# Kernel optimization log

Hardware: AMD Instinct MI355X
Metric: run time of the kernel (lower is better)

## Reference

```python
import jax, jax.numpy as jnp
import numpy as np

N_NODES = 100000
N_EDGES = 600000
DIM = 128
NUM_RELS = 8


def setup_inputs() -> dict:
    key = jax.random.key(0)
    k_x, k_ei, k_et, k_w, k_root = jax.random.split(key, 5)
    x = jax.random.normal(k_x, (N_NODES, DIM), dtype=jnp.float32)
    edge_index = jax.random.randint(k_ei, (2, N_EDGES), 0, N_NODES, dtype=jnp.int64)
    edge_type = jax.random.randint(k_et, (N_EDGES,), 0, NUM_RELS, dtype=jnp.int64)
    # per-relation weights, root weight, bias (as in PyG RGCNConv defaults)
    W = jax.random.normal(k_w, (NUM_RELS, DIM, DIM), dtype=jnp.float32) * 0.05
    W_root = jax.random.normal(k_root, (DIM, DIM), dtype=jnp.float32) * 0.05
    bias = jnp.zeros((DIM,), dtype=jnp.float32)
    return {"x": x, "W": W, "W_root": W_root, "bias": bias,
            "edge_index": edge_index, "edge_type": edge_type}


def reference(x, W, W_root, bias, edge_index, edge_type):
    """RGCNConv (num_bases=None, aggr='mean'):
    out[i] = x[i] @ W_root + bias + sum_r mean_{j in N_r(i)} (x[j] @ W[r])
    """
    src = edge_index[0]
    dst = edge_index[1]
    n = x.shape[0]
    num_rels = W.shape[0]
    x_j = x[src]  # [E, D] gather of source-node features
    out = x @ W_root + bias  # root/self transform
    for r in range(num_rels):  # small fixed relation count
        m = (edge_type == r).astype(x.dtype)  # [E]
        msg = (x_j @ W[r]) * m[:, None]  # [E, D] masked per-relation messages
        agg = jax.ops.segment_sum(msg, dst, num_segments=n)  # [N, D]
        cnt = jax.ops.segment_sum(m, dst, num_segments=n)  # [N]
        out = out + agg / jnp.maximum(cnt, 1.0)[:, None]  # per-relation mean
    return out
```

## Files before the change

kernel.cpp:

```cpp
#include <hip/hip_runtime.h>

#define N_NODES 100000
#define N_EDGES 600000
#define DIM 128
#define NUM_RELS 8
#define NBINS (NUM_RELS * N_NODES)
#define SCAN_NB ((NBINS + 1023) / 1024)
#define XBLOCKS 6250
#define TBLOCKS 576
#define HBLOCKS ((N_EDGES + 255) / 256)

typedef unsigned int u32;
typedef __attribute__((ext_vector_type(8))) short bf16x8;
typedef __attribute__((ext_vector_type(4))) float f32x4;

__device__ __forceinline__ u32 pack2_bf16_rn(float lo, float hi) {
    u32 a = __float_as_uint(lo);
    u32 b = __float_as_uint(hi);
    a += 0x7fffu + ((a >> 16) & 1u);
    b += 0x7fffu + ((b >> 16) & 1u);
    return (a >> 16) | (b & 0xffff0000u);
}

__global__ __launch_bounds__(256) void prep(
    const float* __restrict__ x, uint4* __restrict__ x_bf,
    const float* __restrict__ W, const float* __restrict__ W_root,
    unsigned short* __restrict__ Wt,
    const int* __restrict__ ei, const int* __restrict__ et,
    u32* __restrict__ hist, u32* __restrict__ rank) {
    int b = blockIdx.x, tid = threadIdx.x;
    if (b < XBLOCKS) {
        int t = b * 256 + tid;
        const float4* p = reinterpret_cast<const float4*>(x) + (size_t)t * 2;
        float4 v0 = p[0], v1 = p[1];
        uint4 o;
        o.x = pack2_bf16_rn(v0.x, v0.y);
        o.y = pack2_bf16_rn(v0.z, v0.w);
        o.z = pack2_bf16_rn(v1.x, v1.y);
        o.w = pack2_bf16_rn(v1.z, v1.w);
        x_bf[t] = o;
    } else if (b < XBLOCKS + TBLOCKS) {
        int t = (b - XBLOCKS) * 256 + tid;
        int c  = t >> 14;
        int kn = t & 16383;
        int k = kn >> 7, n = kn & 127;
        float v = (c == 0) ? W_root[kn] : W[(size_t)(c - 1) * DIM * DIM + kn];
        u32 bb = __float_as_uint(v);
        bb += 0x7fffu + ((bb >> 16) & 1u);
        Wt[(size_t)c * 16384 + n * 128 + k] = (unsigned short)(bb >> 16);
    } else {
        int e = (b - XBLOCKS - TBLOCKS) * 256 + tid;
        if (e < N_EDGES) {
            int dst = ei[N_EDGES + e];
            int r   = et[e];
            rank[e] = atomicAdd(&hist[(size_t)dst * NUM_RELS + r], 1u);
        }
    }
}

__global__ __launch_bounds__(256) void scan1(const u32* __restrict__ hist,
                                             u32* __restrict__ bsum) {
    __shared__ u32 sh[256];
    int t = threadIdx.x;
    size_t base = (size_t)blockIdx.x * 1024 + t * 4;
    u32 s = 0;
#pragma unroll
    for (int j = 0; j < 4; ++j) { size_t i = base + j; if (i < NBINS) s += hist[i]; }
    sh[t] = s; __syncthreads();
    for (int off = 128; off > 0; off >>= 1) {
        if (t < off) sh[t] += sh[t + off];
        __syncthreads();
    }
    if (t == 0) bsum[blockIdx.x] = sh[0];
}

__global__ __launch_bounds__(256) void scan2(u32* __restrict__ bsum, int nb) {
    __shared__ u32 sh[256];
    int t = threadIdx.x;
    u32 v[4]; u32 s = 0;
#pragma unroll
    for (int j = 0; j < 4; ++j) { int i = t * 4 + j; v[j] = (i < nb) ? bsum[i] : 0; s += v[j]; }
    sh[t] = s; __syncthreads();
    for (int off = 1; off < 256; off <<= 1) {
        u32 add = (t >= off) ? sh[t - off] : 0;
        __syncthreads();
        sh[t] += add;
        __syncthreads();
    }
    u32 run = (t > 0) ? sh[t - 1] : 0;
#pragma unroll
    for (int j = 0; j < 4; ++j) { int i = t * 4 + j; if (i < nb) bsum[i] = run; run += v[j]; }
}

__global__ __launch_bounds__(256) void scan3(const u32* __restrict__ hist,
                                             const u32* __restrict__ bsum,
                                             u32* __restrict__ starts) {
    __shared__ u32 sh[256];
    int t = threadIdx.x;
    size_t base = (size_t)blockIdx.x * 1024 + t * 4;
    u32 v[4]; u32 s = 0;
#pragma unroll
    for (int j = 0; j < 4; ++j) { size_t i = base + j; v[j] = (i < NBINS) ? hist[i] : 0; s += v[j]; }
    sh[t] = s; __syncthreads();
    for (int off = 1; off < 256; off <<= 1) {
        u32 add = (t >= off) ? sh[t - off] : 0;
        __syncthreads();
        sh[t] += add;
        __syncthreads();
    }
    u32 run = bsum[blockIdx.x] + ((t > 0) ? sh[t - 1] : 0);
#pragma unroll
    for (int j = 0; j < 4; ++j) {
        size_t i = base + j;
        if (i < NBINS) {
            starts[i] = run;
            if (i == NBINS - 1) starts[NBINS] = run + v[j];
            run += v[j];
        }
    }
}

__global__ __launch_bounds__(256) void reorder(const int* __restrict__ ei,
                                               const int* __restrict__ et,
                                               const u32* __restrict__ starts,
                                               const u32* __restrict__ rank,
                                               u32* __restrict__ spk) {
    int e = blockIdx.x * 256 + threadIdx.x;
    if (e >= N_EDGES) return;
    int dst = ei[N_EDGES + e];
    int r   = et[e];
    u32 bin = (u32)((dst & 31) * NUM_RELS + r);
    spk[starts[(size_t)dst * NUM_RELS + r] + rank[e]] = (u32)ei[e] | (bin << 17);
}

#define FLUSH2() do { \
    float sc_ = __builtin_amdgcn_rcpf((float)rcnt); \
    ACC[(u32)cur_bin * 64u + ((((lane >> 2) ^ (((u32)cur_bin >> 3) & 15u)) << 2) | (u32)(lane & 3))] = \
        pack2_bf16_rn(a0 * sc_, a1 * sc_); \
} while (0)

__global__ __launch_bounds__(512, 4) void rgcn_fused(
    const u32*  __restrict__ x32,
    const uint4* __restrict__ x16,
    const uint4* __restrict__ Wt,
    const u32*  __restrict__ starts,
    const u32*  __restrict__ spk,
    const float* __restrict__ bias,
    float* __restrict__ out) {
    extern __shared__ u32 ACC[];
    const int tid = threadIdx.x, w = tid >> 6, lane = tid & 63;
    const int g = lane >> 4, m = lane & 15;
    const int rowbase = blockIdx.x * 32;

    uint4* az = reinterpret_cast<uint4*>(ACC);
#pragma unroll
    for (int i = 0; i < 8; ++i) az[tid + i * 512] = make_uint4(0u, 0u, 0u, 0u);
    __syncthreads();

    {
        const u32 elo = starts[(size_t)blockIdx.x * 256 + w * 32];
        const u32 ehi = starts[(size_t)blockIdx.x * 256 + w * 32 + 32];
        int cur_bin = -1, rcnt = 0;
        float a0 = 0.f, a1 = 0.f;
        for (u32 base = elo; base < ehi; base += 64) {
            const int bn = min(64, (int)(ehi - base));
            u32 pk = 0;
            if (lane < bn) pk = spk[base + lane];
            for (int j0 = 0; j0 < bn; j0 += 8) {
                const int lim = bn - j0;
                u32 v[8];
#pragma unroll
                for (int q = 0; q < 8; ++q) {
                    u32 p = (u32)__shfl((int)pk, j0 + (q < lim ? q : 0));
                    v[q] = x32[(size_t)(p & 0x1FFFFu) * 64 + lane];
                }
#pragma unroll
                for (int q = 0; q < 8; ++q) {
                    if (q < lim) {
                        const u32 p = (u32)__shfl((int)pk, j0 + q);
                        const int b = (int)(p >> 17);
                        if (b != cur_bin) {
                            if (rcnt > 0) FLUSH2();
                            cur_bin = b; a0 = 0.f; a1 = 0.f; rcnt = 0;
                        }
                        const u32 vv = v[q];
                        a0 += __uint_as_float(vv << 16);
                        a1 += __uint_as_float(vv & 0xffff0000u);
                        ++rcnt;
                    }
                }
            }
        }
        if (rcnt > 0) FLUSH2();
    }
    __syncthreads();

    const uint4* ATq = reinterpret_cast<const uint4*>(ACC);
    f32x4 accv[2];
    accv[0] = (f32x4)0.f; accv[1] = (f32x4)0.f;
    union { uint4 u; bf16x8 h; } av, bv;
    const int colg = w * 16 + m;

#pragma unroll
    for (int ks = 0; ks < 4; ++ks) {
        bv.u = Wt[(size_t)colg * 16 + ks * 4 + g];
        bf16x8 bf = bv.h;
#pragma unroll
        for (int mt = 0; mt < 2; ++mt) {
            av.u = x16[(size_t)(rowbase + mt * 16 + m) * 16 + ks * 4 + g];
            accv[mt] = __builtin_amdgcn_mfma_f32_16x16x32_bf16(av.h, bf, accv[mt], 0, 0, 0);
        }
    }

#pragma unroll 1
    for (int r = 0; r < 8; ++r) {
        const uint4* Wc = Wt + (size_t)(r + 1) * 2048;
#pragma unroll
        for (int ks = 0; ks < 4; ++ks) {
            bv.u = Wc[(size_t)colg * 16 + ks * 4 + g];
            bf16x8 bf = bv.h;
#pragma unroll
            for (int mt = 0; mt < 2; ++mt) {
                av.u = ATq[(size_t)((mt * 16 + m) * 8 + r) * 16 + (u32)((ks * 4 + g) ^ m)];
                accv[mt] = __builtin_amdgcn_mfma_f32_16x16x32_bf16(av.h, bf, accv[mt], 0, 0, 0);
            }
        }
    }

    {
        const float bb = bias[colg];
#pragma unroll
        for (int mt = 0; mt < 2; ++mt)
#pragma unroll
            for (int j = 0; j < 4; ++j)
                out[(size_t)(rowbase + mt * 16 + g * 4 + j) * DIM + colg] = accv[mt][j] + bb;
    }
}

extern "C" void kernel_launch(void* const* d_in, const int* in_sizes, int n_in,
                              void* d_out, int out_size, void* d_ws, size_t ws_size,
                              hipStream_t stream) {
    const float* x      = (const float*)d_in[0];
    const float* W      = (const float*)d_in[1];
    const float* W_root = (const float*)d_in[2];
    const float* bias   = (const float*)d_in[3];
    const int*   ei     = (const int*)d_in[4];
    const int*   et     = (const int*)d_in[5];
    float* out = (float*)d_out;

    char* ws = (char*)d_ws;
    uint4*          x_bf   = (uint4*)(ws);
    unsigned short* Wt     = (unsigned short*)(ws + 25600000);
    u32*            starts = (u32*)(ws + 25894912);
    u32*            hist   = (u32*)(ws + 29094928);
    u32*            bsum   = (u32*)(ws + 32294928);
    u32*            rank   = (u32*)(ws + 32299024);
    u32*            spk    = (u32*)(ws + 34699024);

    hipMemsetAsync(hist, 0, (size_t)NBINS * 4, stream);
    prep<<<XBLOCKS + TBLOCKS + HBLOCKS, 256, 0, stream>>>(x, x_bf, W, W_root, Wt, ei, et, hist, rank);
    scan1<<<SCAN_NB, 256, 0, stream>>>(hist, bsum);
    scan2<<<1, 256, 0, stream>>>(bsum, SCAN_NB);
    scan3<<<SCAN_NB, 256, 0, stream>>>(hist, bsum, starts);
    reorder<<<HBLOCKS, 256, 0, stream>>>(ei, et, starts, rank, spk);
    rgcn_fused<<<N_NODES / 32, 512, 65536, stream>>>((const u32*)x_bf, x_bf, (const uint4*)Wt,
                                                     starts, spk, bias, out);
}
```

Before: 230.3 us.

## Halve rows per fused block, merge scan passes, and compute bin starts lazily

The fused aggregation and GEMM kernel now handles 16 rows per block instead of 32. This halves its LDS footprint and lets the launch bounds ask for 8 waves per SIMD, so more blocks can be resident to hide the gather latency. The three-pass scan becomes two: local prefixes plus block sums are written once, and consumers add the block offset on the fly, which removes the separate starts pass and one full read of the histogram. In exchange, each block does half the MFMA work per W fetch, and reorder and the block prologue each do an extra lookup.

```diff
diff --git a/kernel.cpp b/kernel.cpp
--- a/kernel.cpp
+++ b/kernel.cpp
@@ -9,6 +9,11 @@
 #define XBLOCKS 6250
 #define TBLOCKS 576
 #define HBLOCKS ((N_EDGES + 255) / 256)
+
+#define RPB 16
+#define BPB (RPB * NUM_RELS)
+#define FBLOCKS (N_NODES / RPB)
+#define LDS_BYTES ((BPB * 64 + 132) * 4)
 
 typedef unsigned int u32;
 typedef __attribute__((ext_vector_type(8))) short bf16x8;
@@ -58,23 +63,33 @@
     }
 }
 
-__global__ __launch_bounds__(256) void scan1(const u32* __restrict__ hist,
+__global__ __launch_bounds__(256) void scanA(const u32* __restrict__ hist,
+                                             u32* __restrict__ locpre,
                                              u32* __restrict__ bsum) {
     __shared__ u32 sh[256];
     int t = threadIdx.x;
     size_t base = (size_t)blockIdx.x * 1024 + t * 4;
-    u32 s = 0;
-#pragma unroll
-    for (int j = 0; j < 4; ++j) { size_t i = base + j; if (i < NBINS) s += hist[i]; }
+    u32 v[4]; u32 s = 0;
+#pragma unroll
+    for (int j = 0; j < 4; ++j) { size_t i = base + j; v[j] = (i < NBINS) ? hist[i] : 0; s += v[j]; }
     sh[t] = s; __syncthreads();
-    for (int off = 128; off > 0; off >>= 1) {
-        if (t < off) sh[t] += sh[t + off];
-        __syncthreads();
-    }
-    if (t == 0) bsum[blockIdx.x] = sh[0];
-}
-
-__global__ __launch_bounds__(256) void scan2(u32* __restrict__ bsum, int nb) {
+    for (int off = 1; off < 256; off <<= 1) {
+        u32 add = (t >= off) ? sh[t - off] : 0;
+        __syncthreads();
+        sh[t] += add;
+        __syncthreads();
+    }
+    u32 run = (t > 0) ? sh[t - 1] : 0;
+#pragma unroll
+    for (int j = 0; j < 4; ++j) {
+        size_t i = base + j;
+        if (i < NBINS) locpre[i] = run;
+        run += v[j];
+    }
+    if (t == 255) bsum[blockIdx.x] = sh[255];
+}
+
+__global__ __launch_bounds__(256) void scanB(u32* __restrict__ bsum, int nb) {
     __shared__ u32 sh[256];
     int t = threadIdx.x;
     u32 v[4]; u32 s = 0;
@@ -92,45 +107,20 @@
     for (int j = 0; j < 4; ++j) { int i = t * 4 + j; if (i < nb) bsum[i] = run; run += v[j]; }
 }
 
-__global__ __launch_bounds__(256) void scan3(const u32* __restrict__ hist,
-                                             const u32* __restrict__ bsum,
-                                             u32* __restrict__ starts) {
-    __shared__ u32 sh[256];
-    int t = threadIdx.x;
-    size_t base = (size_t)blockIdx.x * 1024 + t * 4;
-    u32 v[4]; u32 s = 0;
-#pragma unroll
-    for (int j = 0; j < 4; ++j) { size_t i = base + j; v[j] = (i < NBINS) ? hist[i] : 0; s += v[j]; }
-    sh[t] = s; __syncthreads();
-    for (int off = 1; off < 256; off <<= 1) {
-        u32 add = (t >= off) ? sh[t - off] : 0;
-        __syncthreads();
-        sh[t] += add;
-        __syncthreads();
-    }
-    u32 run = bsum[blockIdx.x] + ((t > 0) ? sh[t - 1] : 0);
-#pragma unroll
-    for (int j = 0; j < 4; ++j) {
-        size_t i = base + j;
-        if (i < NBINS) {
-            starts[i] = run;
-            if (i == NBINS - 1) starts[NBINS] = run + v[j];
-            run += v[j];
-        }
-    }
-}
-
 __global__ __launch_bounds__(256) void reorder(const int* __restrict__ ei,
                                                const int* __restrict__ et,
-                                               const u32* __restrict__ starts,
+                                               const u32* __restrict__ locpre,
+                                               const u32* __restrict__ bsumx,
                                                const u32* __restrict__ rank,
                                                u32* __restrict__ spk) {
     int e = blockIdx.x * 256 + threadIdx.x;
     if (e >= N_EDGES) return;
     int dst = ei[N_EDGES + e];
     int r   = et[e];
-    u32 bin = (u32)((dst & 31) * NUM_RELS + r);
-    spk[starts[(size_t)dst * NUM_RELS + r] + rank[e]] = (u32)ei[e] | (bin << 17);
+    size_t key = (size_t)dst * NUM_RELS + r;
+    u32 pos = locpre[key] + bsumx[key >> 10] + rank[e];
+    u32 bin = (u32)((dst & (RPB - 1)) * NUM_RELS + r);
+    spk[pos] = (u32)ei[e] | (bin << 17);
 }
 
 #define FLUSH2() do { \
@@ -139,27 +129,33 @@
         pack2_bf16_rn(a0 * sc_, a1 * sc_); \
 } while (0)
 
-__global__ __launch_bounds__(512, 4) void rgcn_fused(
+__global__ __launch_bounds__(512, 8) void rgcn_fused(
     const u32*  __restrict__ x32,
     const uint4* __restrict__ x16,
     const uint4* __restrict__ Wt,
-    const u32*  __restrict__ starts,
+    const u32*  __restrict__ locpre,
+    const u32*  __restrict__ bsumx,
     const u32*  __restrict__ spk,
     const float* __restrict__ bias,
     float* __restrict__ out) {
     extern __shared__ u32 ACC[];
+    u32* BND = ACC + BPB * 64;
     const int tid = threadIdx.x, w = tid >> 6, lane = tid & 63;
     const int g = lane >> 4, m = lane & 15;
-    const int rowbase = blockIdx.x * 32;
+    const int rowbase = blockIdx.x * RPB;
 
     uint4* az = reinterpret_cast<uint4*>(ACC);
 #pragma unroll
-    for (int i = 0; i < 8; ++i) az[tid + i * 512] = make_uint4(0u, 0u, 0u, 0u);
+    for (int i = 0; i < 4; ++i) az[tid + i * 512] = make_uint4(0u, 0u, 0u, 0u);
+    if (tid <= BPB) {
+        u32 idx = (u32)blockIdx.x * BPB + (u32)tid;
+        BND[tid] = (idx >= (u32)NBINS) ? (u32)N_EDGES : (locpre[idx] + bsumx[idx >> 10]);
+    }
     __syncthreads();
 
     {
-        const u32 elo = starts[(size_t)blockIdx.x * 256 + w * 32];
-        const u32 ehi = starts[(size_t)blockIdx.x * 256 + w * 32 + 32];
+        const u32 elo = BND[w * 16];
+        const u32 ehi = BND[w * 16 + 16];
         int cur_bin = -1, rcnt = 0;
         float a0 = 0.f, a1 = 0.f;
         for (u32 base = elo; base < ehi; base += 64) {
@@ -168,24 +164,22 @@
             if (lane < bn) pk = spk[base + lane];
             for (int j0 = 0; j0 < bn; j0 += 8) {
                 const int lim = bn - j0;
-                u32 v[8];
+                u32 pq[8], v[8];
 #pragma unroll
                 for (int q = 0; q < 8; ++q) {
-                    u32 p = (u32)__shfl((int)pk, j0 + (q < lim ? q : 0));
-                    v[q] = x32[(size_t)(p & 0x1FFFFu) * 64 + lane];
+                    pq[q] = (u32)__shfl((int)pk, j0 + (q < lim ? q : 0));
+                    v[q] = x32[(size_t)(pq[q] & 0x1FFFFu) * 64 + lane];
                 }
 #pragma unroll
                 for (int q = 0; q < 8; ++q) {
                     if (q < lim) {
-                        const u32 p = (u32)__shfl((int)pk, j0 + q);
-                        const int b = (int)(p >> 17);
+                        const int b = (int)(pq[q] >> 17);
                         if (b != cur_bin) {
                             if (rcnt > 0) FLUSH2();
                             cur_bin = b; a0 = 0.f; a1 = 0.f; rcnt = 0;
                         }
-                        const u32 vv = v[q];
-                        a0 += __uint_as_float(vv << 16);
-                        a1 += __uint_as_float(vv & 0xffff0000u);
+                        a0 += __uint_as_float(v[q] << 16);
+                        a1 += __uint_as_float(v[q] & 0xffff0000u);
                         ++rcnt;
                     }
                 }
@@ -196,20 +190,15 @@
     __syncthreads();
 
     const uint4* ATq = reinterpret_cast<const uint4*>(ACC);
-    f32x4 accv[2];
-    accv[0] = (f32x4)0.f; accv[1] = (f32x4)0.f;
+    f32x4 accv = (f32x4)0.f;
     union { uint4 u; bf16x8 h; } av, bv;
     const int colg = w * 16 + m;
 
 #pragma unroll
     for (int ks = 0; ks < 4; ++ks) {
         bv.u = Wt[(size_t)colg * 16 + ks * 4 + g];
-        bf16x8 bf = bv.h;
-#pragma unroll
-        for (int mt = 0; mt < 2; ++mt) {
-            av.u = x16[(size_t)(rowbase + mt * 16 + m) * 16 + ks * 4 + g];
-            accv[mt] = __builtin_amdgcn_mfma_f32_16x16x32_bf16(av.h, bf, accv[mt], 0, 0, 0);
-        }
+        av.u = x16[(size_t)(rowbase + m) * 16 + ks * 4 + g];
+        accv = __builtin_amdgcn_mfma_f32_16x16x32_bf16(av.h, bv.h, accv, 0, 0, 0);
     }
 
 #pragma unroll 1
@@ -218,22 +207,16 @@
 #pragma unroll
         for (int ks = 0; ks < 4; ++ks) {
             bv.u = Wc[(size_t)colg * 16 + ks * 4 + g];
-            bf16x8 bf = bv.h;
-#pragma unroll
-            for (int mt = 0; mt < 2; ++mt) {
-                av.u = ATq[(size_t)((mt * 16 + m) * 8 + r) * 16 + (u32)((ks * 4 + g) ^ m)];
-                accv[mt] = __builtin_amdgcn_mfma_f32_16x16x32_bf16(av.h, bf, accv[mt], 0, 0, 0);
-            }
+            av.u = ATq[(size_t)(m * 8 + r) * 16 + (u32)((ks * 4 + g) ^ m)];
+            accv = __builtin_amdgcn_mfma_f32_16x16x32_bf16(av.h, bv.h, accv, 0, 0, 0);
         }
     }
 
     {
         const float bb = bias[colg];
 #pragma unroll
-        for (int mt = 0; mt < 2; ++mt)
-#pragma unroll
-            for (int j = 0; j < 4; ++j)
-                out[(size_t)(rowbase + mt * 16 + g * 4 + j) * DIM + colg] = accv[mt][j] + bb;
+        for (int j = 0; j < 4; ++j)
+            out[(size_t)(rowbase + g * 4 + j) * DIM + colg] = accv[j] + bb;
     }
 }
 
@@ -251,18 +234,17 @@
     char* ws = (char*)d_ws;
     uint4*          x_bf   = (uint4*)(ws);
     unsigned short* Wt     = (unsigned short*)(ws + 25600000);
-    u32*            starts = (u32*)(ws + 25894912);
+    u32*            locpre = (u32*)(ws + 25894912);
     u32*            hist   = (u32*)(ws + 29094928);
-    u32*            bsum   = (u32*)(ws + 32294928);
+    u32*            bsumx  = (u32*)(ws + 32294928);
     u32*            rank   = (u32*)(ws + 32299024);
     u32*            spk    = (u32*)(ws + 34699024);
 
     hipMemsetAsync(hist, 0, (size_t)NBINS * 4, stream);
     prep<<<XBLOCKS + TBLOCKS + HBLOCKS, 256, 0, stream>>>(x, x_bf, W, W_root, Wt, ei, et, hist, rank);
-    scan1<<<SCAN_NB, 256, 0, stream>>>(hist, bsum);
-    scan2<<<1, 256, 0, stream>>>(bsum, SCAN_NB);
-    scan3<<<SCAN_NB, 256, 0, stream>>>(hist, bsum, starts);
-    reorder<<<HBLOCKS, 256, 0, stream>>>(ei, et, starts, rank, spk);
-    rgcn_fused<<<N_NODES / 32, 512, 65536, stream>>>((const u32*)x_bf, x_bf, (const uint4*)Wt,
-                                                     starts, spk, bias, out);
-}
+    scanA<<<SCAN_NB, 256, 0, stream>>>(hist, locpre, bsumx);
+    scanB<<<1, 256, 0, stream>>>(bsumx, SCAN_NB);
+    reorder<<<HBLOCKS, 256, 0, stream>>>(ei, et, locpre, bsumx, rank, spk);
+    rgcn_fused<<<FBLOCKS, 512, LDS_BYTES, stream>>>((const u32*)x_bf, x_bf, (const uint4*)Wt,
+                                                    locpre, bsumx, spk, bias, out);
+}
```

Result: slower. 301.0 us (+30.7%).
